# Optimization experiments

Hardware: AMD Instinct MI355X
Metric: run time of the kernel (lower is better)

## Reference

```python
import jax, jax.numpy as jnp
import numpy as np

ATT_DIM = 128
C = 256
B, H, W = 4, 64, 64


def setup_inputs() -> dict:
    key = jax.random.key(0)
    ks = jax.random.split(key, 6)
    s = 1.0 / np.sqrt(C)
    return {
        "x": jax.random.normal(ks[0], (B, C, H, W), dtype=jnp.float32),
        "Wg": jax.random.normal(ks[1], (ATT_DIM, C), dtype=jnp.float32) * s,
        "Wf": jax.random.normal(ks[2], (ATT_DIM, C), dtype=jnp.float32) * s,
        "Wh": jax.random.normal(ks[3], (ATT_DIM, C), dtype=jnp.float32) * s,
        "Wv": jax.random.normal(ks[4], (C, ATT_DIM), dtype=jnp.float32) * (1.0 / np.sqrt(ATT_DIM)),
        "lambda_att": jax.random.normal(ks[5], (), dtype=jnp.float32),
    }


def reference(x, Wg, Wf, Wh, Wv, lambda_att):
    # x: [B, C, H, W]; 1x1 channels_first convs == channel matmuls
    b, c, h, w = x.shape
    hw = h * w
    d = Wg.shape[0]
    # project and flatten spatial dims -> tokens: [B, HW, d]
    g = jnp.einsum('dc,bchw->bhwd', Wg, x).reshape(b, hw, d)  # query
    f = jnp.einsum('dc,bchw->bhwd', Wf, x).reshape(b, hw, d)  # value
    hh = jnp.einsum('dc,bchw->bhwd', Wh, x).reshape(b, hw, d)  # key
    # keras layers.Attention([g, f, h]): scores = query @ key^T (unscaled),
    # out = softmax(scores) @ value
    scores = jnp.einsum('bqd,bkd->bqk', g, hh)  # [B, HW, HW]
    attw = jax.nn.softmax(scores, axis=-1)
    v = jnp.einsum('bqk,bkd->bqd', attw, f)  # [B, HW, d]
    # back to [B, d, H, W], project to C channels
    v = v.transpose(0, 2, 1).reshape(b, d, h, w)
    v = jnp.einsum('cd,bdhw->bchw', Wv, v)
    return x + lambda_att * v
```

## Files before the change

### kernel.cpp

```cpp
#include <hip/hip_runtime.h>

typedef _Float16 h16;
typedef __attribute__((ext_vector_type(8))) _Float16 half8;
typedef __attribute__((ext_vector_type(4))) _Float16 half4;
typedef __attribute__((ext_vector_type(4))) float f32x4;
typedef unsigned int u32;
typedef unsigned long long u64;

#define LOG2E 1.44269504088896340736f

__device__ __forceinline__ void gl_lds16(const void* g, void* l){
  __builtin_amdgcn_global_load_lds((const __attribute__((address_space(1))) u32*)g,
                                   (__attribute__((address_space(3))) u32*)l, 16, 0, 0);
}
__device__ __forceinline__ f32x4 mfma16(half8 a, half8 b, f32x4 c){
  return __builtin_amdgcn_mfma_f32_16x16x32_f16(a, b, c, 0, 0, 0);
}
__device__ __forceinline__ f32x4 fzero(){
  f32x4 z = {0.f, 0.f, 0.f, 0.f};
  return z;
}
__device__ __forceinline__ half8 cvt8(const float* p){
  half8 r = { (h16)p[0], (h16)p[1], (h16)p[2], (h16)p[3],
              (h16)p[4], (h16)p[5], (h16)p[6], (h16)p[7] };
  return r;
}

__global__ __launch_bounds__(256, 2)
void k_proj(const float* __restrict__ x, const float* __restrict__ Wg32,
            const float* __restrict__ Wh32, const float* __restrict__ Wf32,
            h16* __restrict__ Q, h16* __restrict__ K, h16* __restrict__ Vt){
  __shared__ __align__(16) char Xl[64 * 512];
  int bid = blockIdx.x;
  int b = bid >> 6, p0 = (bid & 63) * 64;
  int tid = threadIdx.x;
  int w = tid >> 6, lane = tid & 63, g4 = lane >> 4, ln = lane & 15;

  #pragma unroll
  for (int pass = 0; pass < 4; ++pass){
    int idx = pass * 256 + tid;
    int c4 = idx >> 4, p4 = idx & 15;
    const float* xp = x + ((size_t)b * 256 + c4 * 4) * 4096 + p0 + p4 * 4;
    float4 v0 = *(const float4*)(xp);
    float4 v1 = *(const float4*)(xp + 4096);
    float4 v2 = *(const float4*)(xp + 8192);
    float4 v3 = *(const float4*)(xp + 12288);
    #pragma unroll
    for (int i = 0; i < 4; ++i){
      int row = p4 * 4 + i;
      half4 v = { (h16)((&v0.x)[i]), (h16)((&v1.x)[i]),
                  (h16)((&v2.x)[i]), (h16)((&v3.x)[i]) };
      *(half4*)&Xl[row * 512 + ((c4 * 8) ^ ((row & 7) << 4))] = v;
    }
  }
  __syncthreads();

  half8 xf[4][8];
  #pragma unroll
  for (int pt = 0; pt < 4; ++pt){
    int p = pt * 16 + ln;
    #pragma unroll
    for (int ks = 0; ks < 8; ++ks)
      xf[pt][ks] = *(const half8*)&Xl[p * 512 + (((ks * 4 + g4) ^ (p & 7)) << 4)];
  }

  const float* Ws0[3] = {Wg32, Wh32, Wf32};
  #pragma unroll
  for (int mat = 0; mat < 3; ++mat){
    const float* Wm = Ws0[mat];
    #pragma unroll
    for (int dtl = 0; dtl < 2; ++dtl){
      int drow = w * 32 + dtl * 16 + ln;
      half8 wf[8];
      #pragma unroll
      for (int ks = 0; ks < 8; ++ks)
        wf[ks] = cvt8(&Wm[(size_t)drow * 256 + ks * 32 + g4 * 8]);
      #pragma unroll
      for (int pt = 0; pt < 4; ++pt){
        f32x4 acc = fzero();
        #pragma unroll
        for (int ks = 0; ks < 8; ++ks)
          acc = mfma16(wf[ks], xf[pt][ks], acc);
        int p = p0 + pt * 16 + ln;
        int dbase = w * 32 + dtl * 16 + g4 * 4;
        if (mat < 2){
          h16* Dst = (mat == 0) ? Q : K;
          half4 v = { (h16)acc[0], (h16)acc[1], (h16)acc[2], (h16)acc[3] };
          *(half4*)&Dst[((size_t)b * 4096 + p) * 128 + dbase] = v;
        } else {
          #pragma unroll
          for (int r = 0; r < 4; ++r)
            Vt[((size_t)b * 128 + dbase + r) * 4096 + p] = (h16)acc[r];
        }
      }
    }
  }
}

__global__ __launch_bounds__(256, 2)
void k_attn(const h16* __restrict__ Q, const h16* __restrict__ K,
            const h16* __restrict__ Vt, h16* __restrict__ Opart,
            float* __restrict__ Mb, float* __restrict__ Lb){
  __shared__ __align__(16) char Kl[2][16384];
  __shared__ __align__(16) char Vl[2][16384];
  __shared__ __align__(16) char Pl[4][4096];

  int bid = blockIdx.x;
  int b = bid >> 7, qb = (bid >> 2) & 31, sp = bid & 3;
  int tid = threadIdx.x;
  int w = tid >> 6, lane = tid & 63, g4 = lane >> 4, ln = lane & 15;
  int q0 = qb * 128 + w * 32;

  half8 qf[2][4];
  #pragma unroll
  for (int qt = 0; qt < 2; ++qt)
    #pragma unroll
    for (int ks = 0; ks < 4; ++ks)
      qf[qt][ks] = *(const half8*)&Q[((size_t)b * 4096 + q0 + qt * 16 + ln) * 128 + ks * 32 + g4 * 8];

  f32x4 acc[2][8];
  #pragma unroll
  for (int qt = 0; qt < 2; ++qt)
    #pragma unroll
    for (int dt = 0; dt < 8; ++dt)
      acc[qt][dt] = fzero();
  float mrow[2] = {-1e30f, -1e30f};
  float lrow[2] = {0.f, 0.f};

  int base0 = sp * 1024;

  auto stage = [&](char* kd, char* vd, int kv0){
    #pragma unroll
    for (int i = 0; i < 4; ++i){
      int off = i * 4096 + w * 1024 + lane * 16;
      int row = off >> 8, c16 = (off >> 4) & 15;
      gl_lds16(&K[((size_t)b * 4096 + kv0 + row) * 128 + ((c16 ^ (row & 7)) << 3)],
               kd + i * 4096 + w * 1024);
    }
    #pragma unroll
    for (int i = 0; i < 4; ++i){
      int off = i * 4096 + w * 1024 + lane * 16;
      int row = off >> 7, c16 = (off >> 4) & 7;
      gl_lds16(&Vt[((size_t)b * 128 + row) * 4096 + kv0 + ((c16 ^ (row & 7)) << 3)],
               vd + i * 4096 + w * 1024);
    }
  };

  stage(&Kl[0][0], &Vl[0][0], base0);
  __syncthreads();

  for (int t2 = 0; t2 < 8; ++t2){
    #pragma unroll
    for (int h = 0; h < 2; ++h){
      int t = t2 * 2 + h;
      int kv0 = base0 + t * 64;
      if ((h == 0) | (t2 < 7))
        stage(&Kl[1 - h][0], &Vl[1 - h][0], kv0 + 64);

      f32x4 s[4][2];
      #pragma unroll
      for (int kt = 0; kt < 4; ++kt)
        #pragma unroll
        for (int qt = 0; qt < 2; ++qt) s[kt][qt] = fzero();
      #pragma unroll
      for (int kt = 0; kt < 4; ++kt){
        int key = kt * 16 + ln;
        #pragma unroll
        for (int ks = 0; ks < 4; ++ks){
          half8 kf = *(const half8*)&Kl[h][key * 256 + (((ks * 4 + g4) ^ (key & 7)) << 4)];
          #pragma unroll
          for (int qt = 0; qt < 2; ++qt)
            s[kt][qt] = mfma16(kf, qf[qt][ks], s[kt][qt]);
        }
      }

      #pragma unroll
      for (int qt = 0; qt < 2; ++qt){
        float mx = -1e30f;
        #pragma unroll
        for (int kt = 0; kt < 4; ++kt)
          #pragma unroll
          for (int r = 0; r < 4; ++r) mx = fmaxf(mx, s[kt][qt][r]);
        mx = fmaxf(mx, __shfl_xor(mx, 16));
        mx = fmaxf(mx, __shfl_xor(mx, 32));
        if (!__all(mx <= mrow[qt] + 8.f)){
          float mnew = fmaxf(mrow[qt], mx);
          float scale = exp2f((mrow[qt] - mnew) * LOG2E);
          lrow[qt] *= scale;
          #pragma unroll
          for (int r = 0; r < 4; ++r){
            float sc = __shfl(scale, g4 * 4 + r);
            #pragma unroll
            for (int dt = 0; dt < 8; ++dt) acc[qt][dt][r] *= sc;
          }
          mrow[qt] = mnew;
        }
        float ps = 0.f;
        int q = qt * 16 + ln;
        #pragma unroll
        for (int kt = 0; kt < 4; ++kt){
          float e0 = exp2f((s[kt][qt][0] - mrow[qt]) * LOG2E);
          float e1 = exp2f((s[kt][qt][1] - mrow[qt]) * LOG2E);
          float e2 = exp2f((s[kt][qt][2] - mrow[qt]) * LOG2E);
          float e3 = exp2f((s[kt][qt][3] - mrow[qt]) * LOG2E);
          ps += (e0 + e1) + (e2 + e3);
          half4 pv = { (h16)e0, (h16)e1, (h16)e2, (h16)e3 };
          *(half4*)&Pl[w][q * 128 + ((kt * 32 + g4 * 8) ^ ((q & 7) << 4))] = pv;
        }
        ps += __shfl_xor(ps, 16);
        ps += __shfl_xor(ps, 32);
        lrow[qt] += ps;
      }

      #pragma unroll
      for (int st = 0; st < 2; ++st){
        half8 pa[2];
        #pragma unroll
        for (int qt = 0; qt < 2; ++qt){
          int q = qt * 16 + ln;
          pa[qt] = *(const half8*)&Pl[w][q * 128 + (((st * 4 + g4) ^ (q & 7)) << 4)];
        }
        #pragma unroll
        for (int dt = 0; dt < 8; ++dt){
          int row = dt * 16 + ln;
          half8 vf = *(const half8*)&Vl[h][row * 128 + (((st * 4 + g4) ^ (row & 7)) << 4)];
          #pragma unroll
          for (int qt = 0; qt < 2; ++qt)
            acc[qt][dt] = mfma16(pa[qt], vf, acc[qt][dt]);
        }
      }

      __syncthreads();
    }
  }

  int pb = (b * 64 + qb * 2 + (w >> 1)) * 4 + sp;
  #pragma unroll
  for (int qt = 0; qt < 2; ++qt){
    float inv = 1.f / lrow[qt];
    #pragma unroll
    for (int r = 0; r < 4; ++r){
      float invr = __shfl(inv, g4 * 4 + r);
      int qloc = (w & 1) * 32 + qt * 16 + g4 * 4 + r;
      #pragma unroll
      for (int dt = 0; dt < 8; ++dt)
        Opart[(size_t)pb * 8192 + qloc * 128 + dt * 16 + ln] = (h16)(acc[qt][dt][r] * invr);
    }
  }
  if (lane < 16){
    #pragma unroll
    for (int qt = 0; qt < 2; ++qt){
      int qloc = (w & 1) * 32 + qt * 16 + lane;
      Mb[pb * 64 + qloc] = mrow[qt];
      Lb[pb * 64 + qloc] = lrow[qt];
    }
  }
}

__global__ __launch_bounds__(256, 2)
void k_oproj(const float* __restrict__ x, const float* __restrict__ Wv32,
             const h16* __restrict__ Opart, const float* __restrict__ Mb,
             const float* __restrict__ Lb, const float* __restrict__ lamp,
             float* __restrict__ y){
  int bid = blockIdx.x;
  int b = bid >> 6, g64 = bid & 63;
  int p0 = g64 * 64;
  int tid = threadIdx.x;
  int w = tid >> 6, lane = tid & 63, g4 = lane >> 4, ln = lane & 15;
  float lam = lamp[0];
  int base = (b * 64 + g64) * 4;

  half8 of[4][4];
  #pragma unroll
  for (int pt = 0; pt < 4; ++pt){
    int p = pt * 16 + ln;
    float m0 = Mb[(base + 0) * 64 + p], m1 = Mb[(base + 1) * 64 + p];
    float m2 = Mb[(base + 2) * 64 + p], m3 = Mb[(base + 3) * 64 + p];
    float mmax = fmaxf(fmaxf(m0, m1), fmaxf(m2, m3));
    float w0 = exp2f((m0 - mmax) * LOG2E) * Lb[(base + 0) * 64 + p];
    float w1 = exp2f((m1 - mmax) * LOG2E) * Lb[(base + 1) * 64 + p];
    float w2 = exp2f((m2 - mmax) * LOG2E) * Lb[(base + 2) * 64 + p];
    float w3 = exp2f((m3 - mmax) * LOG2E) * Lb[(base + 3) * 64 + p];
    float inv = 1.f / (w0 + w1 + w2 + w3);
    w0 *= inv; w1 *= inv; w2 *= inv; w3 *= inv;
    #pragma unroll
    for (int ks = 0; ks < 4; ++ks){
      size_t eo = (size_t)p * 128 + ks * 32 + g4 * 8;
      half8 a0 = *(const half8*)&Opart[(size_t)(base + 0) * 8192 + eo];
      half8 a1 = *(const half8*)&Opart[(size_t)(base + 1) * 8192 + eo];
      half8 a2 = *(const half8*)&Opart[(size_t)(base + 2) * 8192 + eo];
      half8 a3 = *(const half8*)&Opart[(size_t)(base + 3) * 8192 + eo];
      half8 o;
      #pragma unroll
      for (int j = 0; j < 8; ++j)
        o[j] = (h16)(w0 * (float)a0[j] + w1 * (float)a1[j]
                   + w2 * (float)a2[j] + w3 * (float)a3[j]);
      of[pt][ks] = o;
    }
  }

  #pragma unroll
  for (int ctl = 0; ctl < 4; ++ctl){
    int crow = w * 64 + ctl * 16 + ln;
    half8 wf[4];
    #pragma unroll
    for (int ks = 0; ks < 4; ++ks)
      wf[ks] = cvt8(&Wv32[(size_t)crow * 128 + ks * 32 + g4 * 8]);
    #pragma unroll
    for (int pt = 0; pt < 4; ++pt){
      f32x4 a = fzero();
      #pragma unroll
      for (int ks = 0; ks < 4; ++ks) a = mfma16(wf[ks], of[pt][ks], a);
      int p = p0 + pt * 16 + ln;
      int c = w * 64 + ctl * 16 + g4 * 4;
      #pragma unroll
      for (int r = 0; r < 4; ++r){
        size_t idx = ((size_t)b * 256 + c + r) * 4096 + p;
        y[idx] = x[idx] + lam * a[r];
      }
    }
  }
}

extern "C" void kernel_launch(void* const* d_in, const int* in_sizes, int n_in,
                              void* d_out, int out_size, void* d_ws, size_t ws_size,
                              hipStream_t stream) {
  const float* x   = (const float*)d_in[0];
  const float* Wg  = (const float*)d_in[1];
  const float* Wf  = (const float*)d_in[2];
  const float* Wh  = (const float*)d_in[3];
  const float* Wv  = (const float*)d_in[4];
  const float* lam = (const float*)d_in[5];

  h16* Qb    = (h16*)d_ws;
  h16* Kb    = Qb + 2097152;
  h16* Vtb   = Kb + 2097152;
  h16* Opart = Vtb + 2097152;
  float* Mb  = (float*)(Opart + 8388608);
  float* Lb  = Mb + 65536;

  k_proj<<<256, 256, 0, stream>>>(x, Wg, Wh, Wf, Qb, Kb, Vtb);
  k_attn<<<512, 256, 0, stream>>>(Qb, Kb, Vtb, Opart, Mb, Lb);
  k_oproj<<<256, 256, 0, stream>>>(x, Wv, Opart, Mb, Lb, lam, (float*)d_out);
}
```

Before: 177.1 us.

## Fold log2e into Q projection, pre-convert weights to fp16, pack P with cvt_pkrtz

Scales Q by log2(e) at projection time so the attention softmax can call exp2 directly without a multiply per score, and raises the lazy-rescale threshold to match the base-2 units. Adds a small kernel that converts all weights to fp16 once per call, so the projection kernels load half8 vectors instead of converting fp32 per element. P tiles are packed with the pkrtz conversion intrinsic. This adds an extra kernel launch and uses round-toward-zero rounding for P.

```diff
diff --git a/kernel.cpp b/kernel.cpp
--- a/kernel.cpp
+++ b/kernel.cpp
@@ -20,15 +20,23 @@
   f32x4 z = {0.f, 0.f, 0.f, 0.f};
   return z;
 }
-__device__ __forceinline__ half8 cvt8(const float* p){
-  half8 r = { (h16)p[0], (h16)p[1], (h16)p[2], (h16)p[3],
-              (h16)p[4], (h16)p[5], (h16)p[6], (h16)p[7] };
-  return r;
+__device__ __forceinline__ u32 pkrtz(float a, float b){
+  return __builtin_bit_cast(u32, __builtin_amdgcn_cvt_pkrtz(a, b));
+}
+
+__global__ void k_cvtw(const float* __restrict__ Wg, const float* __restrict__ Wf,
+                       const float* __restrict__ Wh, const float* __restrict__ Wv,
+                       h16* __restrict__ o){
+  int i = blockIdx.x * 256 + threadIdx.x;
+  o[i]          = (h16)Wg[i];
+  o[32768 + i]  = (h16)Wf[i];
+  o[65536 + i]  = (h16)Wh[i];
+  o[98304 + i]  = (h16)Wv[i];
 }
 
 __global__ __launch_bounds__(256, 2)
-void k_proj(const float* __restrict__ x, const float* __restrict__ Wg32,
-            const float* __restrict__ Wh32, const float* __restrict__ Wf32,
+void k_proj(const float* __restrict__ x, const h16* __restrict__ Wgb,
+            const h16* __restrict__ Whb, const h16* __restrict__ Wfb,
             h16* __restrict__ Q, h16* __restrict__ K, h16* __restrict__ Vt){
   __shared__ __align__(16) char Xl[64 * 512];
   int bid = blockIdx.x;
@@ -64,17 +72,18 @@
       xf[pt][ks] = *(const half8*)&Xl[p * 512 + (((ks * 4 + g4) ^ (p & 7)) << 4)];
   }
 
-  const float* Ws0[3] = {Wg32, Wh32, Wf32};
+  const h16* Ws0[3] = {Wgb, Whb, Wfb};
   #pragma unroll
   for (int mat = 0; mat < 3; ++mat){
-    const float* Wm = Ws0[mat];
+    const h16* Wm = Ws0[mat];
+    float osc = (mat == 0) ? LOG2E : 1.0f;
     #pragma unroll
     for (int dtl = 0; dtl < 2; ++dtl){
       int drow = w * 32 + dtl * 16 + ln;
       half8 wf[8];
       #pragma unroll
       for (int ks = 0; ks < 8; ++ks)
-        wf[ks] = cvt8(&Wm[(size_t)drow * 256 + ks * 32 + g4 * 8]);
+        wf[ks] = *(const half8*)&Wm[(size_t)drow * 256 + ks * 32 + g4 * 8];
       #pragma unroll
       for (int pt = 0; pt < 4; ++pt){
         f32x4 acc = fzero();
@@ -85,7 +94,8 @@
         int dbase = w * 32 + dtl * 16 + g4 * 4;
         if (mat < 2){
           h16* Dst = (mat == 0) ? Q : K;
-          half4 v = { (h16)acc[0], (h16)acc[1], (h16)acc[2], (h16)acc[3] };
+          half4 v = { (h16)(acc[0] * osc), (h16)(acc[1] * osc),
+                      (h16)(acc[2] * osc), (h16)(acc[3] * osc) };
           *(half4*)&Dst[((size_t)b * 4096 + p) * 128 + dbase] = v;
         } else {
           #pragma unroll
@@ -183,9 +193,9 @@
           for (int r = 0; r < 4; ++r) mx = fmaxf(mx, s[kt][qt][r]);
         mx = fmaxf(mx, __shfl_xor(mx, 16));
         mx = fmaxf(mx, __shfl_xor(mx, 32));
-        if (!__all(mx <= mrow[qt] + 8.f)){
+        if (!__all(mx <= mrow[qt] + 11.5f)){
           float mnew = fmaxf(mrow[qt], mx);
-          float scale = exp2f((mrow[qt] - mnew) * LOG2E);
+          float scale = exp2f(mrow[qt] - mnew);
           lrow[qt] *= scale;
           #pragma unroll
           for (int r = 0; r < 4; ++r){
@@ -199,13 +209,13 @@
         int q = qt * 16 + ln;
         #pragma unroll
         for (int kt = 0; kt < 4; ++kt){
-          float e0 = exp2f((s[kt][qt][0] - mrow[qt]) * LOG2E);
-          float e1 = exp2f((s[kt][qt][1] - mrow[qt]) * LOG2E);
-          float e2 = exp2f((s[kt][qt][2] - mrow[qt]) * LOG2E);
-          float e3 = exp2f((s[kt][qt][3] - mrow[qt]) * LOG2E);
+          float e0 = exp2f(s[kt][qt][0] - mrow[qt]);
+          float e1 = exp2f(s[kt][qt][1] - mrow[qt]);
+          float e2 = exp2f(s[kt][qt][2] - mrow[qt]);
+          float e3 = exp2f(s[kt][qt][3] - mrow[qt]);
           ps += (e0 + e1) + (e2 + e3);
-          half4 pv = { (h16)e0, (h16)e1, (h16)e2, (h16)e3 };
-          *(half4*)&Pl[w][q * 128 + ((kt * 32 + g4 * 8) ^ ((q & 7) << 4))] = pv;
+          u64 v = (u64)pkrtz(e0, e1) | ((u64)pkrtz(e2, e3) << 32);
+          *(u64*)&Pl[w][q * 128 + ((kt * 32 + g4 * 8) ^ ((q & 7) << 4))] = v;
         }
         ps += __shfl_xor(ps, 16);
         ps += __shfl_xor(ps, 32);
@@ -258,7 +268,7 @@
 }
 
 __global__ __launch_bounds__(256, 2)
-void k_oproj(const float* __restrict__ x, const float* __restrict__ Wv32,
+void k_oproj(const float* __restrict__ x, const h16* __restrict__ Wvb,
              const h16* __restrict__ Opart, const float* __restrict__ Mb,
              const float* __restrict__ Lb, const float* __restrict__ lamp,
              float* __restrict__ y){
@@ -277,10 +287,10 @@
     float m0 = Mb[(base + 0) * 64 + p], m1 = Mb[(base + 1) * 64 + p];
     float m2 = Mb[(base + 2) * 64 + p], m3 = Mb[(base + 3) * 64 + p];
     float mmax = fmaxf(fmaxf(m0, m1), fmaxf(m2, m3));
-    float w0 = exp2f((m0 - mmax) * LOG2E) * Lb[(base + 0) * 64 + p];
-    float w1 = exp2f((m1 - mmax) * LOG2E) * Lb[(base + 1) * 64 + p];
-    float w2 = exp2f((m2 - mmax) * LOG2E) * Lb[(base + 2) * 64 + p];
-    float w3 = exp2f((m3 - mmax) * LOG2E) * Lb[(base + 3) * 64 + p];
+    float w0 = exp2f(m0 - mmax) * Lb[(base + 0) * 64 + p];
+    float w1 = exp2f(m1 - mmax) * Lb[(base + 1) * 64 + p];
+    float w2 = exp2f(m2 - mmax) * Lb[(base + 2) * 64 + p];
+    float w3 = exp2f(m3 - mmax) * Lb[(base + 3) * 64 + p];
     float inv = 1.f / (w0 + w1 + w2 + w3);
     w0 *= inv; w1 *= inv; w2 *= inv; w3 *= inv;
     #pragma unroll
@@ -305,7 +315,7 @@
     half8 wf[4];
     #pragma unroll
     for (int ks = 0; ks < 4; ++ks)
-      wf[ks] = cvt8(&Wv32[(size_t)crow * 128 + ks * 32 + g4 * 8]);
+      wf[ks] = *(const half8*)&Wvb[(size_t)crow * 128 + ks * 32 + g4 * 8];
     #pragma unroll
     for (int pt = 0; pt < 4; ++pt){
       f32x4 a = fzero();
@@ -332,14 +342,17 @@
   const float* Wv  = (const float*)d_in[4];
   const float* lam = (const float*)d_in[5];
 
-  h16* Qb    = (h16*)d_ws;
+  h16* Wall  = (h16*)d_ws;
+  h16* Qb    = Wall + 131072;
   h16* Kb    = Qb + 2097152;
   h16* Vtb   = Kb + 2097152;
   h16* Opart = Vtb + 2097152;
   float* Mb  = (float*)(Opart + 8388608);
   float* Lb  = Mb + 65536;
 
-  k_proj<<<256, 256, 0, stream>>>(x, Wg, Wh, Wf, Qb, Kb, Vtb);
+  k_cvtw<<<128, 256, 0, stream>>>(Wg, Wf, Wh, Wv, Wall);
+  k_proj<<<256, 256, 0, stream>>>(x, Wall , Wall + 65536 , Wall + 32768 ,
+                                  Qb, Kb, Vtb);
   k_attn<<<512, 256, 0, stream>>>(Qb, Kb, Vtb, Opart, Mb, Lb);
-  k_oproj<<<256, 256, 0, stream>>>(x, Wv, Opart, Mb, Lb, lam, (float*)d_out);
-}
+  k_oproj<<<256, 256, 0, stream>>>(x, Wall + 98304 , Opart, Mb, Lb, lam, (float*)d_out);
+}
```

Result: faster. 152.0 us (-14.2%).
